# Kernel tuning notes

Measured on AMD Instinct MI355X. Metric: run time of the kernel, lower is better.

The kernel has to match this reference:

```python
import jax, jax.numpy as jnp
import numpy as np

N = 30          # num_nodes
F = 4           # feature_dim
H = 64          # decoder_hidden_dim
TF = 2          # decoder_tf_interval
MIN_VAR = 1e-8
MAX_VAR = 100.0

_pairs = np.array([(i, j) for i in range(N) for j in range(N) if i != j])
RECV = jnp.asarray(_pairs[:, 0])   # [E] receiver node per edge
SEND = jnp.asarray(_pairs[:, 1])   # [E] sender node per edge


def _mlp(x, Ws, bs, softplus=False):
    # Linear->ReLU for all hidden layers, final Linear; optional softplus+clip head
    for W, b in zip(Ws[:-1], bs[:-1]):
        x = jax.nn.relu(x @ W + b)
    x = x @ Ws[-1] + bs[-1]
    if softplus:
        x = jnp.clip(jax.nn.softplus(x), MIN_VAR, MAX_VAR)
    return x


def setup_inputs() -> dict:
    key = jax.random.key(0)
    ks = jax.random.split(key, 20)
    B, S, T = 8, 4, 128
    E = N * (N - 1)

    def lin(k, din, dout):
        s = 1.0 / np.sqrt(din)
        return jax.random.uniform(k, (din, dout), jnp.float32, -s, s)

    inp = {
        'data': jax.random.normal(ks[0], (B, S, T, N, F), jnp.float32),
        'graph': (jax.random.uniform(ks[1], (B * S, E)) > 0.5).astype(jnp.float32),
        # msg_fc: 2F -> H -> H
        'msg_W1': lin(ks[2], 2 * F, H), 'msg_b1': jnp.zeros((H,), jnp.float32),
        'msg_W2': lin(ks[3], H, H),     'msg_b2': jnp.zeros((H,), jnp.float32),
        # mean_fc: H -> H -> H -> F
        'mean_W1': lin(ks[4], H, H), 'mean_b1': jnp.zeros((H,), jnp.float32),
        'mean_W2': lin(ks[5], H, H), 'mean_b2': jnp.zeros((H,), jnp.float32),
        'mean_W3': lin(ks[6], H, F), 'mean_b3': jnp.zeros((F,), jnp.float32),
        # variance_fc: H -> H -> H -> F (softplus + clip)
        'var_W1': lin(ks[7], H, H), 'var_b1': jnp.zeros((H,), jnp.float32),
        'var_W2': lin(ks[8], H, H), 'var_b2': jnp.zeros((H,), jnp.float32),
        'var_W3': lin(ks[9], H, F), 'var_b3': jnp.zeros((F,), jnp.float32),
    }
    return inp


def _single_step(prev, graph, p):
    # prev: [B, C, N, F]; graph: [B, E]
    edge_hidden = jnp.concatenate([prev[:, :, RECV, :], prev[:, :, SEND, :]], axis=-1)  # [B,C,E,2F]
    msg = _mlp(edge_hidden, [p['msg_W1'], p['msg_W2']], [p['msg_b1'], p['msg_b2']])     # [B,C,E,H]
    msg = msg * graph[:, None, :, None]
    B, C = prev.shape[0], prev.shape[1]
    # edge2node: sum messages into receiver nodes (normalize=False)
    agg = jnp.zeros((B, C, N, msg.shape[-1]), msg.dtype).at[:, :, RECV, :].add(msg)     # [B,C,N,H]
    mu = _mlp(agg, [p['mean_W1'], p['mean_W2'], p['mean_W3']],
              [p['mean_b1'], p['mean_b2'], p['mean_b3']])
    var = _mlp(agg, [p['var_W1'], p['var_W2'], p['var_W3']],
               [p['var_b1'], p['var_b2'], p['var_b3']], softplus=True)
    return mu, var


def reference(data, graph, msg_W1, msg_b1, msg_W2, msg_b2,
              mean_W1, mean_b1, mean_W2, mean_b2, mean_W3, mean_b3,
              var_W1, var_b1, var_W2, var_b2, var_W3, var_b3):
    p = dict(msg_W1=msg_W1, msg_b1=msg_b1, msg_W2=msg_W2, msg_b2=msg_b2,
             mean_W1=mean_W1, mean_b1=mean_b1, mean_W2=mean_W2, mean_b2=mean_b2,
             mean_W3=mean_W3, mean_b3=mean_b3,
             var_W1=var_W1, var_b1=var_b1, var_W2=var_W2, var_b2=var_b2,
             var_W3=var_W3, var_b3=var_b3)
    B, S, T, Nn, Ff = data.shape
    x = data.reshape(B * S, T, Nn, Ff)
    prev = x[:, ::TF]                       # teacher-forced anchors, [B*S, C, N, F]
    C = prev.shape[1]
    mus, vars = [], []
    for _ in range(TF):
        mu, var = _single_step(prev, graph, p)
        mus.append(mu)
        vars.append(var)
        prev = mu
    # interleave: out[:, i::TF] = step_i
    mu_pred = jnp.stack(mus, axis=2).reshape(B * S, C * TF, Nn, Ff)[:, :T - 1]
    var_pred = jnp.stack(vars, axis=2).reshape(B * S, C * TF, Nn, Ff)[:, :T - 1]
    mu_pred = mu_pred.reshape(B, S, T - 1, Nn, Ff)
    var_pred = var_pred.reshape(B, S, T - 1, Nn, Ff)
    return mu_pred, var_pred
```

## Files before the change

### kernel.cpp

```cpp
#include <hip/hip_runtime.h>
#include <hip/hip_bf16.h>
#include <hip/hip_fp16.h>

typedef unsigned short u16;
typedef unsigned int u32;
typedef __attribute__((ext_vector_type(4))) short short4v;
typedef __attribute__((ext_vector_type(4))) float f32x4;
typedef __attribute__((ext_vector_type(2))) _Float16 half2v;

#define NN 30
#define FF 4
#define EE 870
#define BSZ 32
#define CC 64
#define TT 128
#define NF 120
#define TSTRIDE 15240
#define OUTHALF 487680
#define AST 68
#define WST 68
#define NSETS 4
#define NCPB 2
#define BPB  8


__device__ __forceinline__ float bf2f(u16 u) {
    union { u32 i; float f; } v; v.i = ((u32)u) << 16; return v.f;
}
__device__ __forceinline__ u16 f2bf_fast(float f) {
    union { float f; u32 u; } v; v.f = f;
    return (u16)((v.u + 0x7FFFu + ((v.u >> 16) & 1u)) >> 16);
}
__device__ __forceinline__ float ldv(const void* p, int idx, int isbf) {
    if (isbf) return bf2f(((const u16*)p)[idx]);
    return ((const float*)p)[idx];
}
__device__ __forceinline__ float softplus_clip(float z) {
    float t = __expf(-fabsf(z));
    float sp = fmaxf(z, 0.f) + __logf(1.f + t);
    return fminf(fmaxf(sp, 1e-8f), 100.f);
}
__device__ __forceinline__ f32x4 MFMA16(short4v a, short4v b, f32x4 c) {
    return __builtin_amdgcn_mfma_f32_16x16x16bf16_1k(a, b, c, 0, 0, 0);
}

__device__ __forceinline__ int probe_isbf(const u16* g, int lane) {
    int hit = (g[2 * lane] == 0x3F80u) | (g[128 + 2 * lane] == 0x3F80u);
    unsigned long long b = __ballot(hit);
    return (b != 0ull) ? 1 : 0;
}

__global__ __launch_bounds__(1024, 4)
void sim_fused(const void* __restrict__ data,
               const void* __restrict__ graph,
               const void* __restrict__ mW1, const void* __restrict__ mB1,
               const void* __restrict__ mW2, const void* __restrict__ mB2,
               const void* __restrict__ aW1, const void* __restrict__ aB1,
               const void* __restrict__ aW2, const void* __restrict__ aB2,
               const void* __restrict__ aW3, const void* __restrict__ aB3,
               const void* __restrict__ vW1, const void* __restrict__ vB1,
               const void* __restrict__ vW2, const void* __restrict__ vB2,
               const void* __restrict__ vW3, const void* __restrict__ vB3,
               void* __restrict__ out)
{
    __shared__ __align__(16) float xN[NSETS][NF];
    __shared__ __align__(16) u32 gmaskS[32];
    __shared__ __align__(16) u16 S[NSETS][32 * AST];
    __shared__ __align__(16) u16 lwM2[64 * WST];
    __shared__ __align__(16) u16 lwH1m[64 * WST];
    __shared__ __align__(16) u16 lwH2m[64 * WST];
    __shared__ __align__(16) u16 lwH1v[64 * WST];
    __shared__ __align__(16) u16 lwH2v[64 * WST];
    __shared__ __align__(16) float biasL[5 * 64];

    const int tid  = threadIdx.x;
    const int lane = tid & 63;
    const int wv   = tid >> 6;
    const int set  = wv >> 2;
    const int swv  = wv & 3;
    const int ln15 = lane & 15;
    const int quad = lane >> 4;
    const int bs   = blockIdx.x / BPB;
    const int bg   = blockIdx.x % BPB;
    const int cg   = bg * NSETS + set;
    const int isbf = probe_isbf((const u16*)graph, lane);

    const bool isMean = (swv < 2);
    const int nb = swv & 1;

    if (tid < 32) gmaskS[tid] = 0u;
    if (tid < 512) {
        int s2 = tid >> 7, row = 30 + ((tid >> 6) & 1);
        S[s2][row * AST + (tid & 63)] = 0;
    }
    __syncthreads();

    if (tid < EE) {
        int i = tid / 29;
        int e = tid - i * 29;
        if (ldv(graph, bs * EE + tid, isbf) > 0.5f)
            atomicOr(&gmaskS[i], 1u << e);
    }
    if (isbf) {
        for (int idx2 = tid; idx2 < 2048; idx2 += 1024) {
            int k = idx2 >> 5, o = (idx2 & 31) * 2;
            int d0 = o * WST + k, d1 = d0 + WST;
            u32 w;
            w = ((const u32*)mW2)[idx2]; lwM2[d0]  = (u16)w; lwM2[d1]  = (u16)(w >> 16);
            w = ((const u32*)aW1)[idx2]; lwH1m[d0] = (u16)w; lwH1m[d1] = (u16)(w >> 16);
            w = ((const u32*)aW2)[idx2]; lwH2m[d0] = (u16)w; lwH2m[d1] = (u16)(w >> 16);
            w = ((const u32*)vW1)[idx2]; lwH1v[d0] = (u16)w; lwH1v[d1] = (u16)(w >> 16);
            w = ((const u32*)vW2)[idx2]; lwH2v[d0] = (u16)w; lwH2v[d1] = (u16)(w >> 16);
        }
    } else {
        for (int idx = tid; idx < 4096; idx += 1024) {
            int k = idx >> 6, o = idx & 63;
            int d = o * WST + k;
            lwM2[d]  = f2bf_fast(((const float*)mW2)[idx]);
            lwH1m[d] = f2bf_fast(((const float*)aW1)[idx]);
            lwH2m[d] = f2bf_fast(((const float*)aW2)[idx]);
            lwH1v[d] = f2bf_fast(((const float*)vW1)[idx]);
            lwH2v[d] = f2bf_fast(((const float*)vW2)[idx]);
        }
    }
    if (tid < 64) {
        biasL[tid]       = ldv(mB2, tid, isbf);
        biasL[64 + tid]  = ldv(aB1, tid, isbf);
        biasL[128 + tid] = ldv(aB2, tid, isbf);
        biasL[192 + tid] = ldv(vB1, tid, isbf);
        biasL[256 + tid] = ldv(vB2, tid, isbf);
    }

    float w1r[8];
#pragma unroll
    for (int k = 0; k < 8; k++) w1r[k] = ldv(mW1, k * 64 + lane, isbf);
    const float b1r = ldv(mB1, lane, isbf);
    float b3r[4];
#pragma unroll
    for (int r = 0; r < 4; r++) b3r[r] = ldv(isMean ? aB3 : vB3, r, isbf);

    const u16* wH1 = isMean ? lwH1m : lwH1v;
    const u16* wH2 = isMean ? lwH2m : lwH2v;
    const float* bAgg = biasL;
    const float* bH1  = isMean ? (biasL + 64)  : (biasL + 192);
    const float* bH2  = isMean ? (biasL + 128) : (biasL + 256);

    const void* W3src = isMean ? aW3 : vW3;
    short4v eA[4];
#pragma unroll
    for (int kb = 0; kb < 4; kb++) {
        union { short4v v; u16 s[4]; } pk;
#pragma unroll
        for (int j = 0; j < 4; j++) {
            int k = kb * 16 + quad * 4 + j;
            pk.s[j] = (ln15 < 4)
                ? (isbf ? ((const u16*)W3src)[k * 4 + ln15]
                        : f2bf_fast(((const float*)W3src)[k * 4 + ln15]))
                : (u16)0;
        }
        eA[kb] = pk.v;
    }

    __syncthreads();

    const int myNode = nb * 16 + ln15;
    const float ngp = (myNode < NN) ? (float)__popc(gmaskS[myNode]) : 0.f;

    auto runLayer = [&](const u16* wl, const float* bl, const short4v* Bin,
                        short4v* Bout, float bscale, bool doRelu) {
#pragma unroll
        for (int fb = 0; fb < 4; fb++) {
            f32x4 acc = {0.f, 0.f, 0.f, 0.f};
#pragma unroll
            for (int kb = 0; kb < 4; kb++) {
                short4v a = *(const short4v*)&wl[(fb * 16 + ln15) * WST + kb * 16 + quad * 4];
                acc = MFMA16(a, Bin[kb], acc);
            }
            float4 bv = *(const float4*)&bl[fb * 16 + quad * 4];
            union { short4v v; u16 s[4]; } pk;
#pragma unroll
            for (int r = 0; r < 4; r++) {
                float val = acc[r] + bscale * (&bv.x)[r];
                if (doRelu) val = fmaxf(val, 0.f);
                pk.s[r] = f2bf_fast(val);
            }
            Bout[fb] = pk.v;
        }
    };

    const int setTid = tid & 255;

    for (int ci = 0; ci < NCPB; ci++) {
        const int c = cg * NCPB + ci;

        if (isbf) {
            if (setTid < 60) {
                u32 w = ((const u32*)data)[((bs * TT + 2 * c) * NF) / 2 + setTid];
                xN[set][setTid * 2]     = bf2f((u16)(w & 0xFFFF));
                xN[set][setTid * 2 + 1] = bf2f((u16)(w >> 16));
            }
        } else {
            if (setTid < NF) xN[set][setTid] = ((const float*)data)[(bs * TT + 2 * c) * NF + setTid];
        }
        __syncthreads();

        for (int step = 0; step < 2; step++) {
            half2v pJp[15];
#pragma unroll
            for (int m = 0; m < 15; m++) {
                float4 xa = *(const float4*)&xN[set][(2 * m) * 4];
                float4 xb = *(const float4*)&xN[set][(2 * m + 1) * 4];
                float pa = xa.x * w1r[4] + xa.y * w1r[5] + xa.z * w1r[6] + xa.w * w1r[7];
                float pb = xb.x * w1r[4] + xb.y * w1r[5] + xb.z * w1r[6] + xb.w * w1r[7];
                half2v p; p.x = (_Float16)pa; p.y = (_Float16)pb;
                pJp[m] = p;
            }

            const half2v zero2 = {(_Float16)0.f, (_Float16)0.f};
            for (int i = swv; i < NN; i += 4) {
                float4 xv = *(const float4*)&xN[set][i * 4];
                float pI = b1r + xv.x * w1r[0] + xv.y * w1r[1] + xv.z * w1r[2] + xv.w * w1r[3];
                _Float16 pih = (_Float16)pI;
                half2v pIp = {pih, pih};
                u32 gm = gmaskS[i];
                u32 lowm = (1u << i) - 1u;
                u32 m2 = __builtin_amdgcn_readfirstlane((gm & lowm) | ((gm & ~lowm) << 1));
                float s0 = 0.f, s1 = 0.f;
#pragma unroll
                for (int m = 0; m < 15; m++) {
                    half2v t = pIp + pJp[m];
                    t = __builtin_elementwise_max(t, zero2);
#if __has_builtin(__builtin_amdgcn_fdot2)
                    u32 mm = ((m2 >> (2 * m)) & 1u) * 0x3C00u
                           + ((m2 >> (2 * m + 1)) & 1u) * 0x3C000000u;
                    half2v mv = __builtin_bit_cast(half2v, mm);
                    if (m & 1) s1 = __builtin_amdgcn_fdot2(t, mv, s1, false);
                    else       s0 = __builtin_amdgcn_fdot2(t, mv, s0, false);
#else
                    u32 mb = ((m2 >> (2 * m)) & 1u) * 0xFFFFu
                           + ((m2 >> (2 * m + 1)) & 1u) * 0xFFFF0000u;
                    u32 tb = __builtin_bit_cast(u32, t) & mb;
                    half2v tv = __builtin_bit_cast(half2v, tb);
                    s0 += (float)tv.x; s1 += (float)tv.y;
#endif
                }
                S[set][i * AST + lane] = f2bf_fast(s0 + s1);
            }
            __syncthreads();

            short4v Bs[4], Ba[4], Bb[4];
#pragma unroll
            for (int kb = 0; kb < 4; kb++)
                Bs[kb] = *(const short4v*)&S[set][(nb * 16 + ln15) * AST + kb * 16 + quad * 4];

            runLayer(lwM2, bAgg, Bs, Ba, ngp, false);
            runLayer(wH1,  bH1,  Ba, Bb, 1.f, true);
            runLayer(wH2,  bH2,  Bb, Ba, 1.f, true);

            {
                f32x4 acc = {0.f, 0.f, 0.f, 0.f};
#pragma unroll
                for (int kb = 0; kb < 4; kb++) acc = MFMA16(eA[kb], Ba[kb], acc);
                const int n = nb * 16 + ln15;
                const int t = 2 * c + step;
                if (quad == 0 && n < NN) {
                    float v[4];
#pragma unroll
                    for (int r = 0; r < 4; r++) v[r] = acc[r] + b3r[r];
                    if (!isMean) {
#pragma unroll
                        for (int r = 0; r < 4; r++) v[r] = softplus_clip(v[r]);
                    }
                    if (t < 127) {
                        size_t o = (size_t)bs * TSTRIDE + (size_t)t * NF + n * 4
                                 + (isMean ? 0 : OUTHALF);
                        if (isbf) {
                            u16* op = (u16*)out;
                            u32 lo = (u32)f2bf_fast(v[0]) | ((u32)f2bf_fast(v[1]) << 16);
                            u32 hi = (u32)f2bf_fast(v[2]) | ((u32)f2bf_fast(v[3]) << 16);
                            *(u32*)&op[o] = lo;
                            *(u32*)&op[o + 2] = hi;
                        } else {
                            float* op = (float*)out;
                            op[o] = v[0]; op[o+1] = v[1]; op[o+2] = v[2]; op[o+3] = v[3];
                        }
                    }
                    if (isMean && step == 0) {
                        xN[set][n*4]   = v[0]; xN[set][n*4+1] = v[1];
                        xN[set][n*4+2] = v[2]; xN[set][n*4+3] = v[3];
                    }
                }
            }
            __syncthreads();
        }
    }
}

extern "C" void kernel_launch(void* const* d_in, const int* in_sizes, int n_in,
                              void* d_out, int out_size, void* d_ws, size_t ws_size,
                              hipStream_t stream) {
    (void)in_sizes; (void)n_in; (void)out_size; (void)d_ws; (void)ws_size;

    const void* data  = d_in[0];
    const void* graph = d_in[1];
    const void* mW1 = d_in[2];  const void* mB1 = d_in[3];
    const void* mW2 = d_in[4];  const void* mB2 = d_in[5];
    const void* aW1 = d_in[6];  const void* aB1 = d_in[7];
    const void* aW2 = d_in[8];  const void* aB2 = d_in[9];
    const void* aW3 = d_in[10]; const void* aB3 = d_in[11];
    const void* vW1 = d_in[12]; const void* vB1 = d_in[13];
    const void* vW2 = d_in[14]; const void* vB2 = d_in[15];
    const void* vW3 = d_in[16]; const void* vB3 = d_in[17];

    sim_fused<<<BSZ * BPB, 1024, 0, stream>>>(data, graph,
        mW1, mB1, mW2, mB2,
        aW1, aB1, aW2, aB2, aW3, aB3,
        vW1, vB1, vW2, vB2, vW3, vB3,
        d_out);
}
```

Before: 134.8 us.

## Process both chunks per set together to halve block barriers

Instead of looping over the two time-chunks each set owns sequentially, the kernel now loads both chunks' anchor states up front and runs the edge-aggregation and MLP stages for both chunks inside each step. This halves the number of __syncthreads per block and interleaves two independent fdot2 accumulation chains for more ILP. In exchange it doubles the S and xN shared buffers and raises register pressure, which under launch_bounds(1024,4) risks spills.

```diff
diff --git a/kernel.cpp b/kernel.cpp
--- a/kernel.cpp
+++ b/kernel.cpp
@@ -63,9 +63,9 @@
                const void* __restrict__ vW3, const void* __restrict__ vB3,
                void* __restrict__ out)
 {
-    __shared__ __align__(16) float xN[NSETS][NF];
+    __shared__ __align__(16) float xN[NSETS][NCPB][NF];
     __shared__ __align__(16) u32 gmaskS[32];
-    __shared__ __align__(16) u16 S[NSETS][32 * AST];
+    __shared__ __align__(16) u16 S[NSETS * NCPB][32 * AST];
     __shared__ __align__(16) u16 lwM2[64 * WST];
     __shared__ __align__(16) u16 lwH1m[64 * WST];
     __shared__ __align__(16) u16 lwH2m[64 * WST];
@@ -89,7 +89,7 @@
     const int nb = swv & 1;
 
     if (tid < 32) gmaskS[tid] = 0u;
-    if (tid < 512) {
+    {
         int s2 = tid >> 7, row = 30 + ((tid >> 6) & 1);
         S[s2][row * AST + (tid & 63)] = 0;
     }
@@ -130,6 +130,23 @@
         biasL[192 + tid] = ldv(vB1, tid, isbf);
         biasL[256 + tid] = ldv(vB2, tid, isbf);
     }
+    {
+        const int setTid = tid & 255;
+#pragma unroll
+        for (int ci = 0; ci < NCPB; ci++) {
+            const int c = cg * NCPB + ci;
+            if (isbf) {
+                if (setTid < 60) {
+                    u32 w = ((const u32*)data)[((bs * TT + 2 * c) * NF) / 2 + setTid];
+                    xN[set][ci][setTid * 2]     = bf2f((u16)(w & 0xFFFF));
+                    xN[set][ci][setTid * 2 + 1] = bf2f((u16)(w >> 16));
+                }
+            } else {
+                if (setTid < NF)
+                    xN[set][ci][setTid] = ((const float*)data)[(bs * TT + 2 * c) * NF + setTid];
+            }
+        }
+    }
 
     float w1r[8];
 #pragma unroll
@@ -188,111 +205,114 @@
         }
     };
 
-    const int setTid = tid & 255;
-
-    for (int ci = 0; ci < NCPB; ci++) {
-        const int c = cg * NCPB + ci;
-
-        if (isbf) {
-            if (setTid < 60) {
-                u32 w = ((const u32*)data)[((bs * TT + 2 * c) * NF) / 2 + setTid];
-                xN[set][setTid * 2]     = bf2f((u16)(w & 0xFFFF));
-                xN[set][setTid * 2 + 1] = bf2f((u16)(w >> 16));
-            }
-        } else {
-            if (setTid < NF) xN[set][setTid] = ((const float*)data)[(bs * TT + 2 * c) * NF + setTid];
-        }
-        __syncthreads();
-
-        for (int step = 0; step < 2; step++) {
-            half2v pJp[15];
+    const half2v zero2 = {(_Float16)0.f, (_Float16)0.f};
+
+    for (int step = 0; step < 2; step++) {
+        {
+            half2v pJp0[15], pJp1[15];
 #pragma unroll
             for (int m = 0; m < 15; m++) {
-                float4 xa = *(const float4*)&xN[set][(2 * m) * 4];
-                float4 xb = *(const float4*)&xN[set][(2 * m + 1) * 4];
-                float pa = xa.x * w1r[4] + xa.y * w1r[5] + xa.z * w1r[6] + xa.w * w1r[7];
-                float pb = xb.x * w1r[4] + xb.y * w1r[5] + xb.z * w1r[6] + xb.w * w1r[7];
-                half2v p; p.x = (_Float16)pa; p.y = (_Float16)pb;
-                pJp[m] = p;
-            }
-
-            const half2v zero2 = {(_Float16)0.f, (_Float16)0.f};
+                float4 xa0 = *(const float4*)&xN[set][0][(2 * m) * 4];
+                float4 xb0 = *(const float4*)&xN[set][0][(2 * m + 1) * 4];
+                float4 xa1 = *(const float4*)&xN[set][1][(2 * m) * 4];
+                float4 xb1 = *(const float4*)&xN[set][1][(2 * m + 1) * 4];
+                half2v p0, p1;
+                p0.x = (_Float16)(xa0.x * w1r[4] + xa0.y * w1r[5] + xa0.z * w1r[6] + xa0.w * w1r[7]);
+                p0.y = (_Float16)(xb0.x * w1r[4] + xb0.y * w1r[5] + xb0.z * w1r[6] + xb0.w * w1r[7]);
+                p1.x = (_Float16)(xa1.x * w1r[4] + xa1.y * w1r[5] + xa1.z * w1r[6] + xa1.w * w1r[7]);
+                p1.y = (_Float16)(xb1.x * w1r[4] + xb1.y * w1r[5] + xb1.z * w1r[6] + xb1.w * w1r[7]);
+                pJp0[m] = p0; pJp1[m] = p1;
+            }
+
             for (int i = swv; i < NN; i += 4) {
-                float4 xv = *(const float4*)&xN[set][i * 4];
-                float pI = b1r + xv.x * w1r[0] + xv.y * w1r[1] + xv.z * w1r[2] + xv.w * w1r[3];
-                _Float16 pih = (_Float16)pI;
-                half2v pIp = {pih, pih};
+                float4 xv0 = *(const float4*)&xN[set][0][i * 4];
+                float4 xv1 = *(const float4*)&xN[set][1][i * 4];
+                float pI0 = b1r + xv0.x * w1r[0] + xv0.y * w1r[1] + xv0.z * w1r[2] + xv0.w * w1r[3];
+                float pI1 = b1r + xv1.x * w1r[0] + xv1.y * w1r[1] + xv1.z * w1r[2] + xv1.w * w1r[3];
+                _Float16 ph0 = (_Float16)pI0, ph1 = (_Float16)pI1;
+                half2v pIp0 = {ph0, ph0}, pIp1 = {ph1, ph1};
                 u32 gm = gmaskS[i];
                 u32 lowm = (1u << i) - 1u;
                 u32 m2 = __builtin_amdgcn_readfirstlane((gm & lowm) | ((gm & ~lowm) << 1));
-                float s0 = 0.f, s1 = 0.f;
+                float s00 = 0.f, s01 = 0.f, s10 = 0.f, s11 = 0.f;
 #pragma unroll
                 for (int m = 0; m < 15; m++) {
-                    half2v t = pIp + pJp[m];
-                    t = __builtin_elementwise_max(t, zero2);
+                    half2v t0 = pIp0 + pJp0[m];
+                    half2v t1 = pIp1 + pJp1[m];
+                    t0 = __builtin_elementwise_max(t0, zero2);
+                    t1 = __builtin_elementwise_max(t1, zero2);
 #if __has_builtin(__builtin_amdgcn_fdot2)
                     u32 mm = ((m2 >> (2 * m)) & 1u) * 0x3C00u
                            + ((m2 >> (2 * m + 1)) & 1u) * 0x3C000000u;
                     half2v mv = __builtin_bit_cast(half2v, mm);
-                    if (m & 1) s1 = __builtin_amdgcn_fdot2(t, mv, s1, false);
-                    else       s0 = __builtin_amdgcn_fdot2(t, mv, s0, false);
+                    if (m & 1) { s01 = __builtin_amdgcn_fdot2(t0, mv, s01, false);
+                                 s11 = __builtin_amdgcn_fdot2(t1, mv, s11, false); }
+                    else       { s00 = __builtin_amdgcn_fdot2(t0, mv, s00, false);
+                                 s10 = __builtin_amdgcn_fdot2(t1, mv, s10, false); }
 #else
                     u32 mb = ((m2 >> (2 * m)) & 1u) * 0xFFFFu
                            + ((m2 >> (2 * m + 1)) & 1u) * 0xFFFF0000u;
-                    u32 tb = __builtin_bit_cast(u32, t) & mb;
-                    half2v tv = __builtin_bit_cast(half2v, tb);
-                    s0 += (float)tv.x; s1 += (float)tv.y;
+                    u32 tb0 = __builtin_bit_cast(u32, t0) & mb;
+                    u32 tb1 = __builtin_bit_cast(u32, t1) & mb;
+                    half2v tv0 = __builtin_bit_cast(half2v, tb0);
+                    half2v tv1 = __builtin_bit_cast(half2v, tb1);
+                    s00 += (float)tv0.x; s01 += (float)tv0.y;
+                    s10 += (float)tv1.x; s11 += (float)tv1.y;
 #endif
                 }
-                S[set][i * AST + lane] = f2bf_fast(s0 + s1);
-            }
-            __syncthreads();
-
+                S[set * NCPB + 0][i * AST + lane] = f2bf_fast(s00 + s01);
+                S[set * NCPB + 1][i * AST + lane] = f2bf_fast(s10 + s11);
+            }
+        }
+        __syncthreads();
+
+#pragma unroll
+        for (int ci = 0; ci < NCPB; ci++) {
+            const u16* Sb = S[set * NCPB + ci];
             short4v Bs[4], Ba[4], Bb[4];
 #pragma unroll
             for (int kb = 0; kb < 4; kb++)
-                Bs[kb] = *(const short4v*)&S[set][(nb * 16 + ln15) * AST + kb * 16 + quad * 4];
+                Bs[kb] = *(const short4v*)&Sb[(nb * 16 + ln15) * AST + kb * 16 + quad * 4];
 
             runLayer(lwM2, bAgg, Bs, Ba, ngp, false);
             runLayer(wH1,  bH1,  Ba, Bb, 1.f, true);
             runLayer(wH2,  bH2,  Bb, Ba, 1.f, true);
 
-            {
-                f32x4 acc = {0.f, 0.f, 0.f, 0.f};
-#pragma unroll
-                for (int kb = 0; kb < 4; kb++) acc = MFMA16(eA[kb], Ba[kb], acc);
-                const int n = nb * 16 + ln15;
-                const int t = 2 * c + step;
-                if (quad == 0 && n < NN) {
-                    float v[4];
-#pragma unroll
-                    for (int r = 0; r < 4; r++) v[r] = acc[r] + b3r[r];
-                    if (!isMean) {
-#pragma unroll
-                        for (int r = 0; r < 4; r++) v[r] = softplus_clip(v[r]);
+            f32x4 acc = {0.f, 0.f, 0.f, 0.f};
+#pragma unroll
+            for (int kb = 0; kb < 4; kb++) acc = MFMA16(eA[kb], Ba[kb], acc);
+            const int n = nb * 16 + ln15;
+            const int c = cg * NCPB + ci;
+            const int t = 2 * c + step;
+            if (quad == 0 && n < NN) {
+                float v[4];
+#pragma unroll
+                for (int r = 0; r < 4; r++) v[r] = acc[r] + b3r[r];
+                if (!isMean) {
+#pragma unroll
+                    for (int r = 0; r < 4; r++) v[r] = softplus_clip(v[r]);
+                }
+                if (t < 127) {
+                    size_t o = (size_t)bs * TSTRIDE + (size_t)t * NF + n * 4
+                             + (isMean ? 0 : OUTHALF);
+                    if (isbf) {
+                        u16* op = (u16*)out;
+                        u32 lo = (u32)f2bf_fast(v[0]) | ((u32)f2bf_fast(v[1]) << 16);
+                        u32 hi = (u32)f2bf_fast(v[2]) | ((u32)f2bf_fast(v[3]) << 16);
+                        *(u32*)&op[o] = lo;
+                        *(u32*)&op[o + 2] = hi;
+                    } else {
+                        float* op = (float*)out;
+                        op[o] = v[0]; op[o+1] = v[1]; op[o+2] = v[2]; op[o+3] = v[3];
                     }
-                    if (t < 127) {
-                        size_t o = (size_t)bs * TSTRIDE + (size_t)t * NF + n * 4
-                                 + (isMean ? 0 : OUTHALF);
-                        if (isbf) {
-                            u16* op = (u16*)out;
-                            u32 lo = (u32)f2bf_fast(v[0]) | ((u32)f2bf_fast(v[1]) << 16);
-                            u32 hi = (u32)f2bf_fast(v[2]) | ((u32)f2bf_fast(v[3]) << 16);
-                            *(u32*)&op[o] = lo;
-                            *(u32*)&op[o + 2] = hi;
-                        } else {
-                            float* op = (float*)out;
-                            op[o] = v[0]; op[o+1] = v[1]; op[o+2] = v[2]; op[o+3] = v[3];
-                        }
-                    }
-                    if (isMean && step == 0) {
-                        xN[set][n*4]   = v[0]; xN[set][n*4+1] = v[1];
-                        xN[set][n*4+2] = v[2]; xN[set][n*4+3] = v[3];
-                    }
-                }
-            }
-            __syncthreads();
-        }
+                }
+                if (isMean && step == 0) {
+                    xN[set][ci][n*4]   = v[0]; xN[set][ci][n*4+1] = v[1];
+                    xN[set][ci][n*4+2] = v[2]; xN[set][ci][n*4+3] = v[3];
+                }
+            }
+        }
+        __syncthreads();
     }
 }
 
```

New measurement: 173.8 us. 1.29x slower.

## Process both time chunks concurrently per wave set instead of sequentially

Applied to the files above, without the earlier changes.

Wave pairs inside each set now each own one chunk index, so both chunks of a set run at the same time. This replaces the sequential chunk loop and removes the extra data-load barriers and per-chunk synchronisations. Each wave now runs both 16-node blocks of the mean or variance MLP rather than one, and the edge-sum loop steps by 2 instead of 4 and uses four fdot2 accumulators for more instruction-level parallelism. The cost is doubled shared-memory buffers for messages and node features, which may limit blocks per CU.

```diff
diff --git a/kernel.cpp b/kernel.cpp
--- a/kernel.cpp
+++ b/kernel.cpp
@@ -63,9 +63,9 @@
                const void* __restrict__ vW3, const void* __restrict__ vB3,
                void* __restrict__ out)
 {
-    __shared__ __align__(16) float xN[NSETS][NF];
+    __shared__ __align__(16) float xN[NSETS][NCPB][NF];
     __shared__ __align__(16) u32 gmaskS[32];
-    __shared__ __align__(16) u16 S[NSETS][32 * AST];
+    __shared__ __align__(16) u16 S[NSETS * NCPB][32 * AST];
     __shared__ __align__(16) u16 lwM2[64 * WST];
     __shared__ __align__(16) u16 lwH1m[64 * WST];
     __shared__ __align__(16) u16 lwH2m[64 * WST];
@@ -77,19 +77,21 @@
     const int lane = tid & 63;
     const int wv   = tid >> 6;
     const int set  = wv >> 2;
-    const int swv  = wv & 3;
+    const int wr   = wv & 3;
+    const int ci   = wr >> 1;
+    const int sub  = wr & 1;
     const int ln15 = lane & 15;
     const int quad = lane >> 4;
     const int bs   = blockIdx.x / BPB;
     const int bg   = blockIdx.x % BPB;
     const int cg   = bg * NSETS + set;
+    const int c    = cg * NCPB + ci;
     const int isbf = probe_isbf((const u16*)graph, lane);
 
-    const bool isMean = (swv < 2);
-    const int nb = swv & 1;
+    const bool isMean = (sub == 0);
 
     if (tid < 32) gmaskS[tid] = 0u;
-    if (tid < 512) {
+    {
         int s2 = tid >> 7, row = 30 + ((tid >> 6) & 1);
         S[s2][row * AST + (tid & 63)] = 0;
     }
@@ -130,6 +132,23 @@
         biasL[192 + tid] = ldv(vB1, tid, isbf);
         biasL[256 + tid] = ldv(vB2, tid, isbf);
     }
+    {
+        const int setTid = tid & 255;
+#pragma unroll
+        for (int cj = 0; cj < NCPB; cj++) {
+            const int cc = cg * NCPB + cj;
+            if (isbf) {
+                if (setTid < 60) {
+                    u32 w = ((const u32*)data)[((bs * TT + 2 * cc) * NF) / 2 + setTid];
+                    xN[set][cj][setTid * 2]     = bf2f((u16)(w & 0xFFFF));
+                    xN[set][cj][setTid * 2 + 1] = bf2f((u16)(w >> 16));
+                }
+            } else {
+                if (setTid < NF)
+                    xN[set][cj][setTid] = ((const float*)data)[(bs * TT + 2 * cc) * NF + setTid];
+            }
+        }
+    }
 
     float w1r[8];
 #pragma unroll
@@ -163,8 +182,8 @@
 
     __syncthreads();
 
-    const int myNode = nb * 16 + ln15;
-    const float ngp = (myNode < NN) ? (float)__popc(gmaskS[myNode]) : 0.f;
+    const float ngpA = (float)__popc(gmaskS[ln15]);
+    const float ngpB = (float)__popc(gmaskS[16 + ln15]);
 
     auto runLayer = [&](const u16* wl, const float* bl, const short4v* Bin,
                         short4v* Bout, float bscale, bool doRelu) {
@@ -188,44 +207,31 @@
         }
     };
 
-    const int setTid = tid & 255;
-
-    for (int ci = 0; ci < NCPB; ci++) {
-        const int c = cg * NCPB + ci;
-
-        if (isbf) {
-            if (setTid < 60) {
-                u32 w = ((const u32*)data)[((bs * TT + 2 * c) * NF) / 2 + setTid];
-                xN[set][setTid * 2]     = bf2f((u16)(w & 0xFFFF));
-                xN[set][setTid * 2 + 1] = bf2f((u16)(w >> 16));
-            }
-        } else {
-            if (setTid < NF) xN[set][setTid] = ((const float*)data)[(bs * TT + 2 * c) * NF + setTid];
-        }
-        __syncthreads();
-
-        for (int step = 0; step < 2; step++) {
+    const half2v zero2 = {(_Float16)0.f, (_Float16)0.f};
+    u16* const Smine = S[set * NCPB + ci];
+
+    for (int step = 0; step < 2; step++) {
+        {
             half2v pJp[15];
 #pragma unroll
             for (int m = 0; m < 15; m++) {
-                float4 xa = *(const float4*)&xN[set][(2 * m) * 4];
-                float4 xb = *(const float4*)&xN[set][(2 * m + 1) * 4];
-                float pa = xa.x * w1r[4] + xa.y * w1r[5] + xa.z * w1r[6] + xa.w * w1r[7];
-                float pb = xb.x * w1r[4] + xb.y * w1r[5] + xb.z * w1r[6] + xb.w * w1r[7];
-                half2v p; p.x = (_Float16)pa; p.y = (_Float16)pb;
+                float4 xa = *(const float4*)&xN[set][ci][(2 * m) * 4];
+                float4 xb = *(const float4*)&xN[set][ci][(2 * m + 1) * 4];
+                half2v p;
+                p.x = (_Float16)(xa.x * w1r[4] + xa.y * w1r[5] + xa.z * w1r[6] + xa.w * w1r[7]);
+                p.y = (_Float16)(xb.x * w1r[4] + xb.y * w1r[5] + xb.z * w1r[6] + xb.w * w1r[7]);
                 pJp[m] = p;
             }
 
-            const half2v zero2 = {(_Float16)0.f, (_Float16)0.f};
-            for (int i = swv; i < NN; i += 4) {
-                float4 xv = *(const float4*)&xN[set][i * 4];
+            for (int i = sub; i < NN; i += 2) {
+                float4 xv = *(const float4*)&xN[set][ci][i * 4];
                 float pI = b1r + xv.x * w1r[0] + xv.y * w1r[1] + xv.z * w1r[2] + xv.w * w1r[3];
                 _Float16 pih = (_Float16)pI;
                 half2v pIp = {pih, pih};
                 u32 gm = gmaskS[i];
                 u32 lowm = (1u << i) - 1u;
                 u32 m2 = __builtin_amdgcn_readfirstlane((gm & lowm) | ((gm & ~lowm) << 1));
-                float s0 = 0.f, s1 = 0.f;
+                float s0 = 0.f, s1 = 0.f, s2 = 0.f, s3 = 0.f;
 #pragma unroll
                 for (int m = 0; m < 15; m++) {
                     half2v t = pIp + pJp[m];
@@ -234,8 +240,10 @@
                     u32 mm = ((m2 >> (2 * m)) & 1u) * 0x3C00u
                            + ((m2 >> (2 * m + 1)) & 1u) * 0x3C000000u;
                     half2v mv = __builtin_bit_cast(half2v, mm);
-                    if (m & 1) s1 = __builtin_amdgcn_fdot2(t, mv, s1, false);
-                    else       s0 = __builtin_amdgcn_fdot2(t, mv, s0, false);
+                    if ((m & 3) == 0)      s0 = __builtin_amdgcn_fdot2(t, mv, s0, false);
+                    else if ((m & 3) == 1) s1 = __builtin_amdgcn_fdot2(t, mv, s1, false);
+                    else if ((m & 3) == 2) s2 = __builtin_amdgcn_fdot2(t, mv, s2, false);
+                    else                   s3 = __builtin_amdgcn_fdot2(t, mv, s3, false);
 #else
                     u32 mb = ((m2 >> (2 * m)) & 1u) * 0xFFFFu
                            + ((m2 >> (2 * m + 1)) & 1u) * 0xFFFF0000u;
@@ -244,55 +252,55 @@
                     s0 += (float)tv.x; s1 += (float)tv.y;
 #endif
                 }
-                S[set][i * AST + lane] = f2bf_fast(s0 + s1);
-            }
-            __syncthreads();
-
+                Smine[i * AST + lane] = f2bf_fast((s0 + s1) + (s2 + s3));
+            }
+        }
+        __syncthreads();
+
+        for (int nb2 = 0; nb2 < 2; ++nb2) {
             short4v Bs[4], Ba[4], Bb[4];
 #pragma unroll
             for (int kb = 0; kb < 4; kb++)
-                Bs[kb] = *(const short4v*)&S[set][(nb * 16 + ln15) * AST + kb * 16 + quad * 4];
-
-            runLayer(lwM2, bAgg, Bs, Ba, ngp, false);
+                Bs[kb] = *(const short4v*)&Smine[((nb2 << 4) + ln15) * AST + kb * 16 + quad * 4];
+
+            runLayer(lwM2, bAgg, Bs, Ba, nb2 ? ngpB : ngpA, false);
             runLayer(wH1,  bH1,  Ba, Bb, 1.f, true);
             runLayer(wH2,  bH2,  Bb, Ba, 1.f, true);
 
-            {
-                f32x4 acc = {0.f, 0.f, 0.f, 0.f};
-#pragma unroll
-                for (int kb = 0; kb < 4; kb++) acc = MFMA16(eA[kb], Ba[kb], acc);
-                const int n = nb * 16 + ln15;
-                const int t = 2 * c + step;
-                if (quad == 0 && n < NN) {
-                    float v[4];
-#pragma unroll
-                    for (int r = 0; r < 4; r++) v[r] = acc[r] + b3r[r];
-                    if (!isMean) {
-#pragma unroll
-                        for (int r = 0; r < 4; r++) v[r] = softplus_clip(v[r]);
+            f32x4 acc = {0.f, 0.f, 0.f, 0.f};
+#pragma unroll
+            for (int kb = 0; kb < 4; kb++) acc = MFMA16(eA[kb], Ba[kb], acc);
+            const int n = (nb2 << 4) + ln15;
+            const int t = 2 * c + step;
+            if (quad == 0 && n < NN) {
+                float v[4];
+#pragma unroll
+                for (int r = 0; r < 4; r++) v[r] = acc[r] + b3r[r];
+                if (!isMean) {
+#pragma unroll
+                    for (int r = 0; r < 4; r++) v[r] = softplus_clip(v[r]);
+                }
+                if (t < 127) {
+                    size_t o = (size_t)bs * TSTRIDE + (size_t)t * NF + n * 4
+                             + (isMean ? 0 : OUTHALF);
+                    if (isbf) {
+                        u16* op = (u16*)out;
+                        u32 lo = (u32)f2bf_fast(v[0]) | ((u32)f2bf_fast(v[1]) << 16);
+                        u32 hi = (u32)f2bf_fast(v[2]) | ((u32)f2bf_fast(v[3]) << 16);
+                        *(u32*)&op[o] = lo;
+                        *(u32*)&op[o + 2] = hi;
+                    } else {
+                        float* op = (float*)out;
+                        op[o] = v[0]; op[o+1] = v[1]; op[o+2] = v[2]; op[o+3] = v[3];
                     }
-                    if (t < 127) {
-                        size_t o = (size_t)bs * TSTRIDE + (size_t)t * NF + n * 4
-                                 + (isMean ? 0 : OUTHALF);
-                        if (isbf) {
-                            u16* op = (u16*)out;
-                            u32 lo = (u32)f2bf_fast(v[0]) | ((u32)f2bf_fast(v[1]) << 16);
-                            u32 hi = (u32)f2bf_fast(v[2]) | ((u32)f2bf_fast(v[3]) << 16);
-                            *(u32*)&op[o] = lo;
-                            *(u32*)&op[o + 2] = hi;
-                        } else {
-                            float* op = (float*)out;
-                            op[o] = v[0]; op[o+1] = v[1]; op[o+2] = v[2]; op[o+3] = v[3];
-                        }
-                    }
-                    if (isMean && step == 0) {
-                        xN[set][n*4]   = v[0]; xN[set][n*4+1] = v[1];
-                        xN[set][n*4+2] = v[2]; xN[set][n*4+3] = v[3];
-                    }
-                }
-            }
-            __syncthreads();
-        }
+                }
+                if (isMean && step == 0) {
+                    xN[set][ci][n*4]   = v[0]; xN[set][ci][n*4+1] = v[1];
+                    xN[set][ci][n*4+2] = v[2]; xN[set][ci][n*4+3] = v[3];
+                }
+            }
+        }
+        __syncthreads();
     }
 }
 
```

Result: slower. 192.3 us (+42.6%).
